# Performance work log

Hardware: AMD Instinct MI355X
Metric: run time of the kernel (lower is better)

Reference implementation:

```python
import jax, jax.numpy as jnp
import numpy as np
from jax import lax

N_LAYER = 4
D_MODEL = 512
N_HEAD = 8
D_HEAD = 64
D_INNER = 2048
KERNEL = 9
POOL = 8
N_CLASSES = 10
BATCH = 4
RAW_LEN = 8192


def setup_inputs() -> dict:
    key = jax.random.key(0)
    ks = jax.random.split(key, 12)
    s = 0.02
    return {
        "signal": jax.random.normal(ks[0], (BATCH, RAW_LEN), jnp.float32),
        "conv_w": jax.random.normal(ks[1], (KERNEL, 1, D_MODEL), jnp.float32) * s,
        "conv_b": jnp.zeros((D_MODEL,), jnp.float32),
        "qkv_w": jax.random.normal(ks[2], (N_LAYER, D_MODEL, 3 * N_HEAD * D_HEAD), jnp.float32) * s,
        "r_w": jax.random.normal(ks[3], (N_LAYER, D_MODEL, N_HEAD * D_HEAD), jnp.float32) * s,
        "o_w": jax.random.normal(ks[4], (N_LAYER, N_HEAD * D_HEAD, D_MODEL), jnp.float32) * s,
        "ff1_w": jax.random.normal(ks[5], (N_LAYER, D_MODEL, D_INNER), jnp.float32) * s,
        "ff1_b": jnp.zeros((N_LAYER, D_INNER), jnp.float32),
        "ff2_w": jax.random.normal(ks[6], (N_LAYER, D_INNER, D_MODEL), jnp.float32) * s,
        "ff2_b": jnp.zeros((N_LAYER, D_MODEL), jnp.float32),
        "r_w_bias": jax.random.normal(ks[7], (N_HEAD, D_HEAD), jnp.float32) * s,
        "r_r_bias": jax.random.normal(ks[8], (N_HEAD, D_HEAD), jnp.float32) * s,
        "fc_w": jax.random.normal(ks[9], (D_MODEL, N_CLASSES), jnp.float32) * s,
        "fc_b": jnp.zeros((N_CLASSES,), jnp.float32),
    }


def _rel_shift(x):
    # x: [qlen, rlen, bsz, n_head]; TF-XL pad/reshape/slice trick
    q, r, b, n = x.shape
    x = jnp.pad(x, ((0, 0), (1, 0), (0, 0), (0, 0)))
    x = x.reshape(r + 1, q, b, n)[1:]
    return x.reshape(q, r, b, n)


def _forward(signal, conv_w, conv_b, qkv_w, r_w, o_w, ff1_w, ff1_b, ff2_w,
             ff2_b, r_w_bias, r_r_bias, fc_w, fc_b):
    # Conv1D (valid) -> ReLU -> AveragePooling1D
    x = signal[:, :, None]  # [B, L, 1]
    x = lax.conv_general_dilated(x, conv_w, (1,), 'VALID',
                                 dimension_numbers=('NWC', 'WIO', 'NWC')) + conv_b
    x = jax.nn.relu(x)
    B, Lp, D = x.shape
    S = Lp // POOL  # Lp is divisible by POOL for our sizes (keras valid pooling)
    x = x[:, :S * POOL].reshape(B, S, POOL, D).mean(axis=2)
    core = x.transpose(1, 0, 2)  # [S, B, D]

    # sinusoidal relative positional embedding, pos_seq = S-1 .. -(S-1)
    pos_seq = jnp.arange(S - 1, -S, -1, dtype=core.dtype)  # [2S-1]
    inv_freq = 1.0 / (10000.0 ** (jnp.arange(0, D, 2, dtype=core.dtype) / D))
    sin_inp = pos_seq[:, None] * inv_freq[None, :]
    pos_emb = jnp.concatenate([jnp.sin(sin_inp), jnp.cos(sin_inp)], -1)  # [2S-1, D]

    scale = 1.0 / np.sqrt(D_HEAD).astype(np.float32)
    for l in range(N_LAYER):
        heads = core @ qkv_w[l]  # [S, B, 3*H*Dh]
        q, k, v = jnp.split(heads, 3, axis=-1)
        q = q.reshape(S, B, N_HEAD, D_HEAD)
        k = k.reshape(S, B, N_HEAD, D_HEAD)
        v = v.reshape(S, B, N_HEAD, D_HEAD)
        rk = (pos_emb @ r_w[l]).reshape(2 * S - 1, N_HEAD, D_HEAD)

        AC = jnp.einsum('ibnd,jbnd->ijbn', q + r_w_bias, k)      # content term
        BD = jnp.einsum('ibnd,jnd->ijbn', q + r_r_bias, rk)      # position term
        BD = _rel_shift(BD)[:, :S]                                # [S, S, B, H]
        attn_prob = jax.nn.softmax((AC + BD) * scale, axis=1)
        attn_vec = jnp.einsum('ijbn,jbnd->ibnd', attn_prob, v)
        attn_out = attn_vec.reshape(S, B, N_HEAD * D_HEAD) @ o_w[l]
        core = core + attn_out

        # position-wise FF with residual
        h = jax.nn.relu(core @ ff1_w[l] + ff1_b[l]) @ ff2_w[l] + ff2_b[l]
        core = core + h

    # classification head on last timestep
    return core[-1] @ fc_w + fc_b  # [B, n_classes]


def reference(signal, conv_w, conv_b, qkv_w, r_w, o_w, ff1_w, ff1_b, ff2_w,
              ff2_b, r_w_bias, r_r_bias, fc_w, fc_b):
    return _forward(signal, conv_w, conv_b, qkv_w, r_w, o_w, ff1_w, ff1_b,
                    ff2_w, ff2_b, r_w_bias, r_r_bias, fc_w, fc_b)
```

## Files before the change

kernel.cpp:

```cpp
#include <hip/hip_runtime.h>
#include <math.h>

#define S_LEN   1023
#define BATCH_N 4
#define DMODEL  512
#define NHEAD   8
#define DHEAD   64
#define DINNER  2048
#define NLAYER  4
#define RAWLEN  8192
#define POOLW   8
#define KERNW   9
#define RLEN    (2*S_LEN-1)
#define MROWS   (S_LEN*BATCH_N)

using bf16x8 = __attribute__((ext_vector_type(8))) short;
using f32x4  = __attribute__((ext_vector_type(4))) float;

__device__ __forceinline__ unsigned short f2bf(float f) {
    union { float f; unsigned int u; } v; v.f = f;
    unsigned int u = v.u;
    return (unsigned short)((u + 0x7fffu + ((u >> 16) & 1u)) >> 16);
}
__device__ __forceinline__ float bf2f(unsigned short h) {
    union { unsigned int u; float f; } v; v.u = ((unsigned int)h) << 16;
    return v.f;
}

__device__ __forceinline__ void gload_lds16(const void* g, void* l) {
    using gvoid = const __attribute__((address_space(1))) void;
    using lvoid = __attribute__((address_space(3))) void;
    gvoid* gp = reinterpret_cast<gvoid*>(reinterpret_cast<unsigned long long>(g));
    lvoid* lp = reinterpret_cast<lvoid*>((unsigned int)reinterpret_cast<unsigned long long>(l));
    __builtin_amdgcn_global_load_lds(gp, lp, 16, 0, 0);
}

__global__ __launch_bounds__(512) void conv_pool_kernel(
    const float* __restrict__ sig, const float* __restrict__ cw,
    const float* __restrict__ cb, float* __restrict__ core,
    unsigned short* __restrict__ core_bf)
{
    int s = blockIdx.x, b = blockIdx.y, d = threadIdx.x;
    __shared__ float sseg[POOLW + KERNW - 1];
    if (d < POOLW + KERNW - 1) sseg[d] = sig[b*RAWLEN + s*POOLW + d];
    __syncthreads();
    float w[KERNW];
#pragma unroll
    for (int k = 0; k < KERNW; k++) w[k] = cw[k*DMODEL + d];
    float bias = cb[d];
    float acc = 0.f;
#pragma unroll
    for (int p = 0; p < POOLW; p++) {
        float c = bias;
#pragma unroll
        for (int k = 0; k < KERNW; k++) c = fmaf(sseg[p+k], w[k], c);
        acc += fmaxf(c, 0.f);
    }
    float v = acc * (1.0f/POOLW);
    core[(s*BATCH_N + b)*DMODEL + d] = v;
    core_bf[(s*BATCH_N + b)*DMODEL + d] = f2bf(v);
}

__global__ __launch_bounds__(512) void posemb_kernel(unsigned short* __restrict__ pe)
{
    int j = blockIdx.x, d = threadIdx.x;
    float pos = (float)(S_LEN - 1 - j);
    int i = (d < 256) ? d : d - 256;
    float invf = exp2f(-(float)i * (13.287712f/256.0f));
    float a = pos * invf;
    pe[j*DMODEL + d] = f2bf((d < 256) ? __sinf(a) : __cosf(a));
}

__global__ __launch_bounds__(256) void transpose_all_kernel(
    const float* __restrict__ qw, const float* __restrict__ rw,
    const float* __restrict__ ow, const float* __restrict__ f1,
    const float* __restrict__ f2,
    unsigned short* __restrict__ qT, unsigned short* __restrict__ rT,
    unsigned short* __restrict__ oT, unsigned short* __restrict__ f1T,
    unsigned short* __restrict__ f2T)
{
    int id = blockIdx.x;
    const float* W; unsigned short* Wt; int K, N, bx, by;
    if (id < 768)       { W = qw;  Wt = qT;  K = 512;  N = 1536; bx = id % 48; by = id / 48; }
    else if (id < 1024) { id -= 768;  W = rw;  Wt = rT;  K = 512;  N = 512;  bx = id % 16; by = id / 16; }
    else if (id < 1280) { id -= 1024; W = ow;  Wt = oT;  K = 512;  N = 512;  bx = id % 16; by = id / 16; }
    else if (id < 2304) { id -= 1280; W = f1;  Wt = f1T; K = 512;  N = 2048; bx = id % 64; by = id / 64; }
    else                { id -= 2304; W = f2;  Wt = f2T; K = 2048; N = 512;  bx = id % 16; by = id / 16; }

    __shared__ float L[32][33];
    int n0 = bx*32, k0 = by*32;
    int t = threadIdx.x;
    int kk = t>>3, nq = (t&7)*4;
    float4 v = *reinterpret_cast<const float4*>(&W[(size_t)(k0+kk)*N + n0 + nq]);
    L[kk][nq+0]=v.x; L[kk][nq+1]=v.y; L[kk][nq+2]=v.z; L[kk][nq+3]=v.w;
    __syncthreads();
    int nn = t>>3, kq = (t&7)*4;
    ushort4 o;
    o.x = f2bf(L[kq+0][nn]); o.y = f2bf(L[kq+1][nn]);
    o.z = f2bf(L[kq+2][nn]); o.w = f2bf(L[kq+3][nn]);
    *reinterpret_cast<ushort4*>(&Wt[(size_t)(n0+nn)*K + k0 + kq]) = o;
}

template<int BN, bool ACCUM, bool BIAS, bool RELU, bool WF32, bool WBF>
__global__ __launch_bounds__(256) void gemm_mfma(
    const unsigned short* __restrict__ A, const unsigned short* __restrict__ Bt,
    const float* __restrict__ bias, float* __restrict__ C,
    unsigned short* __restrict__ Cb, int M, int N, int K)
{
    constexpr int MF = (BN == 128) ? 4 : 2;
    __shared__ unsigned short As[128*32];
    __shared__ unsigned short Bs[BN*32];
    int bm = blockIdx.y * 128, bn = blockIdx.x * BN;
    int tid = threadIdx.x, lane = tid & 63, wid = tid >> 6;

    f32x4 acc[MF][4];
#pragma unroll
    for (int m=0;m<MF;m++)
#pragma unroll
        for (int n=0;n<4;n++) acc[m][n] = (f32x4){0.f,0.f,0.f,0.f};

    int r0 = wid*16 + (lane>>2);
    int slot = (lane&3)*8;
    int ga0 = bm + r0;      if (ga0 > M-1) ga0 = M-1;
    int ga1 = bm + r0 + 64; if (ga1 > M-1) ga1 = M-1;
    const unsigned short* pA0 = A  + (size_t)ga0*K + slot;
    const unsigned short* pA1 = A  + (size_t)ga1*K + slot;
    const unsigned short* pB0 = Bt + (size_t)(bn + r0)*K + slot;
    const unsigned short* pB1 = (BN==128) ? Bt + (size_t)(bn + r0 + 64)*K + slot : nullptr;
    char* lA0 = (char*)As + wid*1024;
    char* lA1 = (char*)As + (wid+4)*1024;
    char* lB0 = (char*)Bs + wid*1024;
    char* lB1 = (char*)Bs + (wid+4)*1024;

    int ar = (BN==128 ? (wid>>1)*64 : wid*32) + (lane&15);
    int br = (BN==128 ? (wid&1)*64 : 0) + (lane&15);
    int kc = (lane>>4)*8;

    for (int k0 = 0; k0 < K; k0 += 32) {
        __syncthreads();
        gload_lds16(pA0, lA0);
        gload_lds16(pA1, lA1);
        gload_lds16(pB0, lB0);
        if (BN == 128) gload_lds16(pB1, lB1);
        pA0 += 32; pA1 += 32; pB0 += 32; if (BN==128) pB1 += 32;
        __syncthreads();
        bf16x8 a[MF], b[4];
#pragma unroll
        for (int m=0;m<MF;m++) a[m] = *reinterpret_cast<const bf16x8*>(&As[(ar + m*16)*32 + kc]);
#pragma unroll
        for (int n=0;n<4;n++) b[n] = *reinterpret_cast<const bf16x8*>(&Bs[(br + n*16)*32 + kc]);
#pragma unroll
        for (int m=0;m<MF;m++)
#pragma unroll
            for (int n=0;n<4;n++)
                acc[m][n] = __builtin_amdgcn_mfma_f32_16x16x32_bf16(a[m], b[n], acc[m][n], 0,0,0);
    }

    int col0 = bn + (BN==128 ? (wid&1)*64 : 0) + (lane&15);
    int rbase = bm + (BN==128 ? (wid>>1)*64 : wid*32) + (lane>>4)*4;
#pragma unroll
    for (int m=0;m<MF;m++) {
#pragma unroll
        for (int n=0;n<4;n++) {
            int col = col0 + n*16;
            float bv = BIAS ? bias[col] : 0.f;
#pragma unroll
            for (int r=0;r<4;r++) {
                int row = rbase + m*16 + r;
                if (row < M) {
                    float v = acc[m][n][r] + bv;
                    if (RELU) v = fmaxf(v, 0.f);
                    size_t off = (size_t)row*N + col;
                    if (ACCUM) v += C[off];
                    if (WF32) C[off] = v;
                    if (WBF)  Cb[off] = f2bf(v);
                }
            }
        }
    }
}

template<bool ACCUM, bool BIAS, bool RELU, bool WF32, bool WBF>
__global__ __launch_bounds__(256) void gemm_mfma64(
    const unsigned short* __restrict__ A, const unsigned short* __restrict__ Bt,
    const float* __restrict__ bias, float* __restrict__ C,
    unsigned short* __restrict__ Cb, int M, int N, int K)
{
    __shared__ unsigned short As[64*32];
    __shared__ unsigned short Bs[64*32];
    int bm = blockIdx.y * 64, bn = blockIdx.x * 64;
    int tid = threadIdx.x, lane = tid & 63, wid = tid >> 6;
    int wr = wid >> 1, wc = wid & 1;

    f32x4 acc[2][2];
#pragma unroll
    for (int m=0;m<2;m++)
#pragma unroll
        for (int n=0;n<2;n++) acc[m][n] = (f32x4){0.f,0.f,0.f,0.f};

    int r0 = wid*16 + (lane>>2);
    int slot = (lane&3)*8;
    int ga = bm + r0; if (ga > M-1) ga = M-1;
    const unsigned short* pA = A  + (size_t)ga*K + slot;
    const unsigned short* pB = Bt + (size_t)(bn + r0)*K + slot;
    char* lA = (char*)As + wid*1024;
    char* lB = (char*)Bs + wid*1024;

    int ar = wr*32 + (lane&15);
    int br = wc*32 + (lane&15);
    int kc = (lane>>4)*8;

    for (int k0 = 0; k0 < K; k0 += 32) {
        __syncthreads();
        gload_lds16(pA, lA);
        gload_lds16(pB, lB);
        pA += 32; pB += 32;
        __syncthreads();
        bf16x8 a[2], b[2];
#pragma unroll
        for (int m=0;m<2;m++) a[m] = *reinterpret_cast<const bf16x8*>(&As[(ar + m*16)*32 + kc]);
#pragma unroll
        for (int n=0;n<2;n++) b[n] = *reinterpret_cast<const bf16x8*>(&Bs[(br + n*16)*32 + kc]);
#pragma unroll
        for (int m=0;m<2;m++)
#pragma unroll
            for (int n=0;n<2;n++)
                acc[m][n] = __builtin_amdgcn_mfma_f32_16x16x32_bf16(a[m], b[n], acc[m][n], 0,0,0);
    }

    int col0 = bn + wc*32 + (lane&15);
    int rbase = bm + wr*32 + (lane>>4)*4;
#pragma unroll
    for (int m=0;m<2;m++) {
#pragma unroll
        for (int n=0;n<2;n++) {
            int col = col0 + n*16;
            float bv = BIAS ? bias[col] : 0.f;
#pragma unroll
            for (int r=0;r<4;r++) {
                int row = rbase + m*16 + r;
                if (row < M) {
                    float v = acc[m][n][r] + bv;
                    if (RELU) v = fmaxf(v, 0.f);
                    size_t off = (size_t)row*N + col;
                    if (ACCUM) v += C[off];
                    if (WF32) C[off] = v;
                    if (WBF)  Cb[off] = f2bf(v);
                }
            }
        }
    }
}

#define TI 16
#define TJ 32
#define PSTR 40
#define ACSTR 36
#define BDSTR 68

__global__ __launch_bounds__(256) void attn_mfma_kernel(
    const unsigned short* __restrict__ heads,
    const unsigned short* __restrict__ rk,
    const float* __restrict__ rwb, const float* __restrict__ rrb,
    unsigned short* __restrict__ av)
{
    int i0 = blockIdx.x * TI;
    int bn = blockIdx.y; int b = bn >> 3, n = bn & 7;
    int tid = threadIdx.x, lane = tid & 63, wid = tid >> 6;
    int kc = (lane>>4)*8;
    int l15 = lane & 15;

    __shared__ float Sac[TI*ACSTR];
    __shared__ float Sbd[TI*BDSTR];
    __shared__ unsigned short Pb[TI*PSTR];
    __shared__ float mrow[TI], lrow[TI], frow[TI];

    const int base0 = (S_LEN-1) - i0 - (TI-1);

    bf16x8 qwf0, qwf1, qrf0, qrf1;
    {
        int gi = i0 + l15; if (gi > S_LEN-1) gi = S_LEN-1;
        const unsigned short* qb = heads + (size_t)(gi*BATCH_N + b)*1536 + n*64;
        bf16x8 u0 = *reinterpret_cast<const bf16x8*>(qb + kc);
        bf16x8 u1 = *reinterpret_cast<const bf16x8*>(qb + 32 + kc);
#pragma unroll
        for (int e=0;e<8;e++) {
            float f0 = bf2f((unsigned short)u0[e]);
            float f1 = bf2f((unsigned short)u1[e]);
            qwf0[e] = (short)f2bf(f0 + rwb[n*64 + kc + e]);
            qrf0[e] = (short)f2bf(f0 + rrb[n*64 + kc + e]);
            qwf1[e] = (short)f2bf(f1 + rwb[n*64 + 32 + kc + e]);
            qrf1[e] = (short)f2bf(f1 + rrb[n*64 + 32 + kc + e]);
        }
    }
    if (tid < TI) { mrow[tid] = -1e30f; lrow[tid] = 0.f; }

    f32x4 Oa = (f32x4){0.f,0.f,0.f,0.f};
    int rw = (lane>>4)*4;

    for (int t = 0; t < 32; t++) {
        int j0 = t * TJ;
        __syncthreads();

        if (wid < 2) {
            int gj = j0 + wid*16 + l15; if (gj > S_LEN-1) gj = S_LEN-1;
            const unsigned short* kb = heads + (size_t)(gj*BATCH_N + b)*1536 + 512 + n*64;
            bf16x8 kf0 = *reinterpret_cast<const bf16x8*>(kb + kc);
            bf16x8 kf1 = *reinterpret_cast<const bf16x8*>(kb + 32 + kc);
            f32x4 s = (f32x4){0.f,0.f,0.f,0.f};
            s = __builtin_amdgcn_mfma_f32_16x16x32_bf16(qwf0, kf0, s, 0,0,0);
            s = __builtin_amdgcn_mfma_f32_16x16x32_bf16(qwf1, kf1, s, 0,0,0);
            int ci = wid*16 + l15;
#pragma unroll
            for (int r=0;r<4;r++) Sac[(rw+r)*ACSTR + ci] = s[r];
        } else if (t == 0) {
            int bh = wid - 2;
#pragma unroll
            for (int q=0;q<2;q++) {
                int w = (bh + q*2)*16 + l15;
                int gr = base0 + w; gr = gr < 0 ? 0 : (gr > RLEN-1 ? RLEN-1 : gr);
                const unsigned short* rb = rk + (size_t)gr*DMODEL + n*64;
                bf16x8 rf0 = *reinterpret_cast<const bf16x8*>(rb + kc);
                bf16x8 rf1 = *reinterpret_cast<const bf16x8*>(rb + 32 + kc);
                f32x4 sb = (f32x4){0.f,0.f,0.f,0.f};
                sb = __builtin_amdgcn_mfma_f32_16x16x32_bf16(qrf0, rf0, sb, 0,0,0);
                sb = __builtin_amdgcn_mfma_f32_16x16x32_bf16(qrf1, rf1, sb, 0,0,0);
#pragma unroll
                for (int r=0;r<4;r++) Sbd[(rw+r)*BDSTR + w] = sb[r];
            }
        } else {
            int bh = wid - 2;
            int pblk = ((t & 1) ? 0 : 2) + bh;
            int w = pblk*16 + l15;
            int off = 32*(t+1) + (w & 31);
            int gr = base0 + off; gr = gr < 0 ? 0 : (gr > RLEN-1 ? RLEN-1 : gr);
            const unsigned short* rb = rk + (size_t)gr*DMODEL + n*64;
            bf16x8 rf0 = *reinterpret_cast<const bf16x8*>(rb + kc);
            bf16x8 rf1 = *reinterpret_cast<const bf16x8*>(rb + 32 + kc);
            f32x4 sb = (f32x4){0.f,0.f,0.f,0.f};
            sb = __builtin_amdgcn_mfma_f32_16x16x32_bf16(qrf0, rf0, sb, 0,0,0);
            sb = __builtin_amdgcn_mfma_f32_16x16x32_bf16(qrf1, rf1, sb, 0,0,0);
#pragma unroll
            for (int r=0;r<4;r++) Sbd[(rw+r)*BDSTR + w] = sb[r];
        }
        __syncthreads();

        {
            int r = tid >> 4, sg = tid & 15, jl = sg*2;
            float a0 = Sac[r*ACSTR + jl], a1 = Sac[r*ACSTR + jl + 1];
            int cb2 = 32*t + (TI-1) - r;
            float s0 = (a0 + Sbd[r*BDSTR + ((cb2+jl  )&63)]) * 0.125f;
            float s1 = (a1 + Sbd[r*BDSTR + ((cb2+jl+1)&63)]) * 0.125f;
            int jg = j0 + jl;
            if (jg+0 >= S_LEN) s0 = -1e30f;
            if (jg+1 >= S_LEN) s1 = -1e30f;
            float tm = fmaxf(s0, s1);
            tm = fmaxf(tm, __shfl_xor(tm, 1));
            tm = fmaxf(tm, __shfl_xor(tm, 2));
            tm = fmaxf(tm, __shfl_xor(tm, 4));
            tm = fmaxf(tm, __shfl_xor(tm, 8));
            float mo = mrow[r];
            float mnew = fmaxf(mo, tm);
            float f = __expf(mo - mnew);
            float e0 = __expf(s0 - mnew), e1 = __expf(s1 - mnew);
            float ssum = e0 + e1;
            ssum += __shfl_xor(ssum, 1);
            ssum += __shfl_xor(ssum, 2);
            ssum += __shfl_xor(ssum, 4);
            ssum += __shfl_xor(ssum, 8);
            if (sg == 0) {
                mrow[r] = mnew;
                lrow[r] = lrow[r]*f + ssum;
                frow[r] = f;
            }
            *reinterpret_cast<ushort2*>(&Pb[r*PSTR + jl]) =
                make_ushort2(f2bf(e0), f2bf(e1));
        }
        __syncthreads();

        {
            float f0 = frow[rw+0], f1 = frow[rw+1], f2 = frow[rw+2], f3 = frow[rw+3];
            Oa[0] *= f0; Oa[1] *= f1; Oa[2] *= f2; Oa[3] *= f3;
            bf16x8 pf = *reinterpret_cast<const bf16x8*>(&Pb[l15*PSTR + kc]);
            int d = wid*16 + l15;
            const unsigned short* vb = heads + 1024 + n*64 + d;
            bf16x8 vf;
#pragma unroll
            for (int e=0;e<8;e++) {
                int gj = j0 + kc + e; if (gj > S_LEN-1) gj = S_LEN-1;
                vf[e] = (short)vb[(size_t)(gj*BATCH_N + b)*1536];
            }
            Oa = __builtin_amdgcn_mfma_f32_16x16x32_bf16(pf, vf, Oa, 0,0,0);
        }
    }
    __syncthreads();

    {
        int d = wid*16 + l15;
#pragma unroll
        for (int r=0;r<4;r++) {
            int gi = i0 + rw + r;
            if (gi < S_LEN) {
                float o = Oa[r] / lrow[rw + r];
                av[(size_t)(gi*BATCH_N + b)*DMODEL + n*64 + d] = f2bf(o);
            }
        }
    }
}

__global__ __launch_bounds__(64) void final_kernel(
    const float* __restrict__ core, const float* __restrict__ fcw,
    const float* __restrict__ fcb, float* __restrict__ out)
{
    int idx = blockIdx.x;
    int b = idx / 10, c = idx % 10;
    int lane = threadIdx.x;
    const float* row = &core[(size_t)((S_LEN-1)*BATCH_N + b)*DMODEL];
    float acc = 0.f;
    for (int d = lane; d < DMODEL; d += 64)
        acc = fmaf(row[d], fcw[d*10 + c], acc);
#pragma unroll
    for (int off = 32; off; off >>= 1) acc += __shfl_xor(acc, off);
    if (lane == 0) out[b*10 + c] = acc + fcb[c];
}

extern "C" void kernel_launch(void* const* d_in, const int* in_sizes, int n_in,
                              void* d_out, int out_size, void* d_ws, size_t ws_size,
                              hipStream_t stream)
{
    const float* sig   = (const float*)d_in[0];
    const float* cw    = (const float*)d_in[1];
    const float* cb    = (const float*)d_in[2];
    const float* qkv_w = (const float*)d_in[3];
    const float* r_w   = (const float*)d_in[4];
    const float* o_w   = (const float*)d_in[5];
    const float* ff1_w = (const float*)d_in[6];
    const float* ff1_b = (const float*)d_in[7];
    const float* ff2_w = (const float*)d_in[8];
    const float* ff2_b = (const float*)d_in[9];
    const float* rwb   = (const float*)d_in[10];
    const float* rrb   = (const float*)d_in[11];
    const float* fcw   = (const float*)d_in[12];
    const float* fcb   = (const float*)d_in[13];
    float* out = (float*)d_out;

    float* core = (float*)d_ws;
    unsigned short* core_bf = (unsigned short*)(core + (size_t)MROWS*DMODEL);
    unsigned short* pe_bf   = core_bf + (size_t)MROWS*DMODEL;
    unsigned short* rk_bf   = pe_bf   + (size_t)RLEN*DMODEL;
    unsigned short* av_bf   = rk_bf   + (size_t)RLEN*DMODEL;
    unsigned short* big_bf  = av_bf   + (size_t)MROWS*DMODEL;
    unsigned short* qkvT = big_bf + (size_t)MROWS*DINNER;
    unsigned short* rwT  = qkvT + (size_t)(3*DMODEL)*DMODEL;
    unsigned short* owT  = rwT  + (size_t)DMODEL*DMODEL;
    unsigned short* ff1T = owT  + (size_t)DMODEL*DMODEL;
    unsigned short* ff2T = ff1T + (size_t)DINNER*DMODEL;

    conv_pool_kernel<<<dim3(S_LEN, BATCH_N), 512, 0, stream>>>(sig, cw, cb, core, core_bf);
    posemb_kernel<<<RLEN, 512, 0, stream>>>(pe_bf);

    for (int l = 0; l < NLAYER; l++) {
        transpose_all_kernel<<<3328, 256, 0, stream>>>(
            qkv_w + (size_t)l*DMODEL*(3*DMODEL),
            r_w   + (size_t)l*DMODEL*DMODEL,
            o_w   + (size_t)l*DMODEL*DMODEL,
            ff1_w + (size_t)l*DMODEL*DINNER,
            ff2_w + (size_t)l*DINNER*DMODEL,
            qkvT, rwT, owT, ff1T, ff2T);

        gemm_mfma<64,false,false,false,false,true><<<dim3(24,32), 256, 0, stream>>>(
            core_bf, qkvT, nullptr, nullptr, big_bf, MROWS, 3*DMODEL, DMODEL);
        gemm_mfma64<false,false,false,false,true><<<dim3(8,32), 256, 0, stream>>>(
            pe_bf, rwT, nullptr, nullptr, rk_bf, RLEN, DMODEL, DMODEL);
        attn_mfma_kernel<<<dim3(64,32), 256, 0, stream>>>(big_bf, rk_bf, rwb, rrb, av_bf);
        gemm_mfma64<true,false,false,true,true><<<dim3(8,64), 256, 0, stream>>>(
            av_bf, owT, nullptr, core, core_bf, MROWS, DMODEL, DMODEL);
        gemm_mfma<128,false,true,true,false,true><<<dim3(16,32), 256, 0, stream>>>(
            core_bf, ff1T, ff1_b + (size_t)l*DINNER, nullptr, big_bf, MROWS, DINNER, DMODEL);
        gemm_mfma64<true,true,false,true,true><<<dim3(8,64), 256, 0, stream>>>(
            big_bf, ff2T, ff2_b + (size_t)l*DMODEL, core, core_bf, MROWS, DMODEL, DINNER);
    }

    final_kernel<<<40, 64, 0, stream>>>(core, fcw, fcb, out);
}
```

Before: 825.4 us.

## Give each wavefront its own 16 query rows in attention, removing block barriers

The attention kernel now assigns each of the four wavefronts an independent 16-row query tile, so each block covers 64 queries and the grid shrinks by four. Softmax running max and sum move from shared memory into registers. Block-wide __syncthreads calls are replaced with per-wave LDS waits. Each wave now computes the full content and position score tiles and all four 16-column output slices itself, which removes cross-wave synchronisation. The trade-off is more registers per thread, fewer blocks in the grid, and redundant strided V loads per wave.

```diff
diff --git a/kernel.cpp b/kernel.cpp
--- a/kernel.cpp
+++ b/kernel.cpp
@@ -252,11 +252,8 @@
     }
 }
 
-#define TI 16
-#define TJ 32
-#define PSTR 40
-#define ACSTR 36
-#define BDSTR 68
+#define AQSTR 68
+#define APSTR 40
 
 __global__ __launch_bounds__(256) void attn_mfma_kernel(
     const unsigned short* __restrict__ heads,
@@ -264,22 +261,23 @@
     const float* __restrict__ rwb, const float* __restrict__ rrb,
     unsigned short* __restrict__ av)
 {
-    int i0 = blockIdx.x * TI;
     int bn = blockIdx.y; int b = bn >> 3, n = bn & 7;
     int tid = threadIdx.x, lane = tid & 63, wid = tid >> 6;
+    int iw0 = blockIdx.x * 64 + wid * 16;
+    int l15 = lane & 15;
     int kc = (lane>>4)*8;
-    int l15 = lane & 15;
-
-    __shared__ float Sac[TI*ACSTR];
-    __shared__ float Sbd[TI*BDSTR];
-    __shared__ unsigned short Pb[TI*PSTR];
-    __shared__ float mrow[TI], lrow[TI], frow[TI];
-
-    const int base0 = (S_LEN-1) - i0 - (TI-1);
+    int rw = (lane>>4)*4;
+
+    __shared__ float SbdA[4*16*AQSTR];
+    __shared__ unsigned short PbA[4*16*APSTR];
+    float* Sbd = &SbdA[wid*16*AQSTR];
+    unsigned short* Pb = &PbA[wid*16*APSTR];
+
+    const int base0 = (S_LEN-1) - iw0 - 15;
 
     bf16x8 qwf0, qwf1, qrf0, qrf1;
     {
-        int gi = i0 + l15; if (gi > S_LEN-1) gi = S_LEN-1;
+        int gi = iw0 + l15; if (gi > S_LEN-1) gi = S_LEN-1;
         const unsigned short* qb = heads + (size_t)(gi*BATCH_N + b)*1536 + n*64;
         bf16x8 u0 = *reinterpret_cast<const bf16x8*>(qb + kc);
         bf16x8 u1 = *reinterpret_cast<const bf16x8*>(qb + 32 + kc);
@@ -293,31 +291,33 @@
             qrf1[e] = (short)f2bf(f1 + rrb[n*64 + 32 + kc + e]);
         }
     }
-    if (tid < TI) { mrow[tid] = -1e30f; lrow[tid] = 0.f; }
-
-    f32x4 Oa = (f32x4){0.f,0.f,0.f,0.f};
-    int rw = (lane>>4)*4;
+
+    float m[4] = {-1e30f,-1e30f,-1e30f,-1e30f};
+    float l[4] = {0.f,0.f,0.f,0.f};
+    f32x4 Oa[4];
+#pragma unroll
+    for (int nn=0;nn<4;nn++) Oa[nn] = (f32x4){0.f,0.f,0.f,0.f};
 
     for (int t = 0; t < 32; t++) {
-        int j0 = t * TJ;
-        __syncthreads();
-
-        if (wid < 2) {
-            int gj = j0 + wid*16 + l15; if (gj > S_LEN-1) gj = S_LEN-1;
+        int j0 = t * 32;
+
+        f32x4 ac[2];
+#pragma unroll
+        for (int c=0;c<2;c++) {
+            int gj = j0 + c*16 + l15; if (gj > S_LEN-1) gj = S_LEN-1;
             const unsigned short* kb = heads + (size_t)(gj*BATCH_N + b)*1536 + 512 + n*64;
             bf16x8 kf0 = *reinterpret_cast<const bf16x8*>(kb + kc);
             bf16x8 kf1 = *reinterpret_cast<const bf16x8*>(kb + 32 + kc);
             f32x4 s = (f32x4){0.f,0.f,0.f,0.f};
             s = __builtin_amdgcn_mfma_f32_16x16x32_bf16(qwf0, kf0, s, 0,0,0);
             s = __builtin_amdgcn_mfma_f32_16x16x32_bf16(qwf1, kf1, s, 0,0,0);
-            int ci = wid*16 + l15;
-#pragma unroll
-            for (int r=0;r<4;r++) Sac[(rw+r)*ACSTR + ci] = s[r];
-        } else if (t == 0) {
-            int bh = wid - 2;
-#pragma unroll
-            for (int q=0;q<2;q++) {
-                int w = (bh + q*2)*16 + l15;
+            ac[c] = s;
+        }
+
+        if (t == 0) {
+#pragma unroll
+            for (int q=0;q<4;q++) {
+                int w = q*16 + l15;
                 int gr = base0 + w; gr = gr < 0 ? 0 : (gr > RLEN-1 ? RLEN-1 : gr);
                 const unsigned short* rb = rk + (size_t)gr*DMODEL + n*64;
                 bf16x8 rf0 = *reinterpret_cast<const bf16x8*>(rb + kc);
@@ -326,83 +326,87 @@
                 sb = __builtin_amdgcn_mfma_f32_16x16x32_bf16(qrf0, rf0, sb, 0,0,0);
                 sb = __builtin_amdgcn_mfma_f32_16x16x32_bf16(qrf1, rf1, sb, 0,0,0);
 #pragma unroll
-                for (int r=0;r<4;r++) Sbd[(rw+r)*BDSTR + w] = sb[r];
+                for (int r=0;r<4;r++) Sbd[(rw+r)*AQSTR + w] = sb[r];
             }
         } else {
-            int bh = wid - 2;
-            int pblk = ((t & 1) ? 0 : 2) + bh;
-            int w = pblk*16 + l15;
-            int off = 32*(t+1) + (w & 31);
-            int gr = base0 + off; gr = gr < 0 ? 0 : (gr > RLEN-1 ? RLEN-1 : gr);
-            const unsigned short* rb = rk + (size_t)gr*DMODEL + n*64;
-            bf16x8 rf0 = *reinterpret_cast<const bf16x8*>(rb + kc);
-            bf16x8 rf1 = *reinterpret_cast<const bf16x8*>(rb + 32 + kc);
-            f32x4 sb = (f32x4){0.f,0.f,0.f,0.f};
-            sb = __builtin_amdgcn_mfma_f32_16x16x32_bf16(qrf0, rf0, sb, 0,0,0);
-            sb = __builtin_amdgcn_mfma_f32_16x16x32_bf16(qrf1, rf1, sb, 0,0,0);
-#pragma unroll
-            for (int r=0;r<4;r++) Sbd[(rw+r)*BDSTR + w] = sb[r];
-        }
-        __syncthreads();
-
-        {
-            int r = tid >> 4, sg = tid & 15, jl = sg*2;
-            float a0 = Sac[r*ACSTR + jl], a1 = Sac[r*ACSTR + jl + 1];
-            int cb2 = 32*t + (TI-1) - r;
-            float s0 = (a0 + Sbd[r*BDSTR + ((cb2+jl  )&63)]) * 0.125f;
-            float s1 = (a1 + Sbd[r*BDSTR + ((cb2+jl+1)&63)]) * 0.125f;
-            int jg = j0 + jl;
-            if (jg+0 >= S_LEN) s0 = -1e30f;
-            if (jg+1 >= S_LEN) s1 = -1e30f;
+#pragma unroll
+            for (int q=0;q<2;q++) {
+                int pblk = ((t & 1) ? 0 : 2) + q;
+                int w = pblk*16 + l15;
+                int off = 32*(t+1) + (w & 31);
+                int gr = base0 + off; gr = gr < 0 ? 0 : (gr > RLEN-1 ? RLEN-1 : gr);
+                const unsigned short* rb = rk + (size_t)gr*DMODEL + n*64;
+                bf16x8 rf0 = *reinterpret_cast<const bf16x8*>(rb + kc);
+                bf16x8 rf1 = *reinterpret_cast<const bf16x8*>(rb + 32 + kc);
+                f32x4 sb = (f32x4){0.f,0.f,0.f,0.f};
+                sb = __builtin_amdgcn_mfma_f32_16x16x32_bf16(qrf0, rf0, sb, 0,0,0);
+                sb = __builtin_amdgcn_mfma_f32_16x16x32_bf16(qrf1, rf1, sb, 0,0,0);
+#pragma unroll
+                for (int r=0;r<4;r++) Sbd[(rw+r)*AQSTR + w] = sb[r];
+            }
+        }
+        asm volatile("s_waitcnt lgkmcnt(0)" ::: "memory");
+        __builtin_amdgcn_sched_barrier(0);
+
+        float fr[4];
+#pragma unroll
+        for (int r=0;r<4;r++) {
+            int row = rw + r;
+            int cb2 = 32*t + 15 - row;
+            float s0 = (ac[0][r] + Sbd[row*AQSTR + ((cb2 + l15)      & 63)]) * 0.125f;
+            float s1 = (ac[1][r] + Sbd[row*AQSTR + ((cb2 + l15 + 16) & 63)]) * 0.125f;
+            if (j0 + l15      >= S_LEN) s0 = -1e30f;
+            if (j0 + l15 + 16 >= S_LEN) s1 = -1e30f;
             float tm = fmaxf(s0, s1);
             tm = fmaxf(tm, __shfl_xor(tm, 1));
             tm = fmaxf(tm, __shfl_xor(tm, 2));
             tm = fmaxf(tm, __shfl_xor(tm, 4));
             tm = fmaxf(tm, __shfl_xor(tm, 8));
-            float mo = mrow[r];
-            float mnew = fmaxf(mo, tm);
-            float f = __expf(mo - mnew);
-            float e0 = __expf(s0 - mnew), e1 = __expf(s1 - mnew);
-            float ssum = e0 + e1;
-            ssum += __shfl_xor(ssum, 1);
-            ssum += __shfl_xor(ssum, 2);
-            ssum += __shfl_xor(ssum, 4);
-            ssum += __shfl_xor(ssum, 8);
-            if (sg == 0) {
-                mrow[r] = mnew;
-                lrow[r] = lrow[r]*f + ssum;
-                frow[r] = f;
-            }
-            *reinterpret_cast<ushort2*>(&Pb[r*PSTR + jl]) =
-                make_ushort2(f2bf(e0), f2bf(e1));
-        }
-        __syncthreads();
+            float mnew = fmaxf(m[r], tm);
+            float fk = __expf(m[r] - mnew);
+            float p0 = __expf(s0 - mnew), p1 = __expf(s1 - mnew);
+            float ss = p0 + p1;
+            ss += __shfl_xor(ss, 1);
+            ss += __shfl_xor(ss, 2);
+            ss += __shfl_xor(ss, 4);
+            ss += __shfl_xor(ss, 8);
+            l[r] = l[r]*fk + ss;
+            m[r] = mnew;
+            fr[r] = fk;
+            Pb[row*APSTR + l15]      = f2bf(p0);
+            Pb[row*APSTR + l15 + 16] = f2bf(p1);
+        }
+        asm volatile("s_waitcnt lgkmcnt(0)" ::: "memory");
+        __builtin_amdgcn_sched_barrier(0);
 
         {
-            float f0 = frow[rw+0], f1 = frow[rw+1], f2 = frow[rw+2], f3 = frow[rw+3];
-            Oa[0] *= f0; Oa[1] *= f1; Oa[2] *= f2; Oa[3] *= f3;
-            bf16x8 pf = *reinterpret_cast<const bf16x8*>(&Pb[l15*PSTR + kc]);
-            int d = wid*16 + l15;
-            const unsigned short* vb = heads + 1024 + n*64 + d;
-            bf16x8 vf;
-#pragma unroll
-            for (int e=0;e<8;e++) {
-                int gj = j0 + kc + e; if (gj > S_LEN-1) gj = S_LEN-1;
-                vf[e] = (short)vb[(size_t)(gj*BATCH_N + b)*1536];
-            }
-            Oa = __builtin_amdgcn_mfma_f32_16x16x32_bf16(pf, vf, Oa, 0,0,0);
-        }
-    }
-    __syncthreads();
-
-    {
-        int d = wid*16 + l15;
-#pragma unroll
-        for (int r=0;r<4;r++) {
-            int gi = i0 + rw + r;
-            if (gi < S_LEN) {
-                float o = Oa[r] / lrow[rw + r];
-                av[(size_t)(gi*BATCH_N + b)*DMODEL + n*64 + d] = f2bf(o);
+            bf16x8 pf = *reinterpret_cast<const bf16x8*>(&Pb[l15*APSTR + kc]);
+            f32x4 fv = (f32x4){fr[0], fr[1], fr[2], fr[3]};
+            const unsigned short* vb = heads + 1024 + n*64;
+#pragma unroll
+            for (int nn=0;nn<4;nn++) {
+                int d = nn*16 + l15;
+                bf16x8 vf;
+#pragma unroll
+                for (int e=0;e<8;e++) {
+                    int gj = j0 + kc + e; if (gj > S_LEN-1) gj = S_LEN-1;
+                    vf[e] = (short)vb[(size_t)(gj*BATCH_N + b)*1536 + d];
+                }
+                Oa[nn] = Oa[nn] * fv;
+                Oa[nn] = __builtin_amdgcn_mfma_f32_16x16x32_bf16(pf, vf, Oa[nn], 0,0,0);
+            }
+        }
+    }
+
+#pragma unroll
+    for (int r=0;r<4;r++) {
+        int gi = iw0 + rw + r;
+        if (gi < S_LEN) {
+            float inv = 1.0f / l[r];
+#pragma unroll
+            for (int nn=0;nn<4;nn++) {
+                av[(size_t)(gi*BATCH_N + b)*DMODEL + n*64 + nn*16 + l15] =
+                    f2bf(Oa[nn][r] * inv);
             }
         }
     }
@@ -472,7 +476,7 @@
             core_bf, qkvT, nullptr, nullptr, big_bf, MROWS, 3*DMODEL, DMODEL);
         gemm_mfma64<false,false,false,false,true><<<dim3(8,32), 256, 0, stream>>>(
             pe_bf, rwT, nullptr, nullptr, rk_bf, RLEN, DMODEL, DMODEL);
-        attn_mfma_kernel<<<dim3(64,32), 256, 0, stream>>>(big_bf, rk_bf, rwb, rrb, av_bf);
+        attn_mfma_kernel<<<dim3(16,32), 256, 0, stream>>>(big_bf, rk_bf, rwb, rrb, av_bf);
         gemm_mfma64<true,false,false,true,true><<<dim3(8,64), 256, 0, stream>>>(
             av_bf, owT, nullptr, core, core_bf, MROWS, DMODEL, DMODEL);
         gemm_mfma<128,false,true,true,false,true><<<dim3(16,32), 256, 0, stream>>>(
```

Result: faster. 767.8 us (-7.0%).
